# Optimization experiments

Measured on AMD Instinct MI355X. Metric: run time of the kernel, lower is better.

Reference implementation:

```python
import jax, jax.numpy as jnp
import numpy as np

B, G, N, C = 8, 16, 1024, 256


def setup_inputs() -> dict:
    key = jax.random.key(0)
    k1, k2, k3, k4, k5 = jax.random.split(key, 5)
    x = jax.random.normal(k1, (B, G, N, C), dtype=jnp.float32)
    vs = jax.random.normal(k2, (B, G, 1, N, 3), dtype=jnp.float32)
    s = 1.0 / np.sqrt(C)
    W_fc = jax.random.normal(k3, (C, C), dtype=jnp.float32) * s   # nn.Linear weight [out,in]
    b_fc = jax.random.normal(k4, (C,), dtype=jnp.float32) * s
    W_vn = jax.random.normal(k5, (C, C), dtype=jnp.float32) * s   # VNLinear weight [out,in], no bias
    return {"x": x, "vs": vs, "W_fc": W_fc, "b_fc": b_fc, "W_vn": W_vn}


def reference(x, vs, W_fc, b_fc, W_vn):
    # q = fc(x): [B,G,N,C]
    q = jnp.einsum('bgnc,oc->bgno', x, W_fc) + b_fc
    # softmax over the point dim N (torch dim=2)
    atten = jax.nn.softmax(q, axis=2)
    xw = atten * x  # [B,G,N,C]
    # torch: expand to [B,G,C,N,3] * vs then sum over N.
    # Equivalent contraction without materializing the 5D tensor:
    v = jnp.squeeze(vs, axis=2)  # [B,G,N,3]
    out = jnp.einsum('bgnc,bgnd->bgcd', xw, v)  # [B,G,C,3]
    # VNLinear: bias-free linear over channel dim, shared across the 3 vector comps
    return jnp.einsum('bgcd,oc->bgod', out, W_vn)  # [B,G,C,3]
```

## Files before the change

### kernel.cpp

```cpp
#include <hip/hip_runtime.h>
#include <hip/hip_bf16.h>


#define NQ 1024
#define CQ 256
#define RT 32
#define TILES 8
#define WB_OFF 131072

typedef __attribute__((ext_vector_type(8))) short bf16x8;
typedef __attribute__((ext_vector_type(4))) float f32x4;

__device__ __forceinline__ ushort2 pk2(float a, float b) {
    __hip_bfloat162 h = __float22bfloat162_rn(make_float2(a, b));
    ushort2 r;
    __builtin_memcpy(&r, &h, sizeof(r));
    return r;
}

__device__ __forceinline__ void gload16(const float* g, float* l) {
    __builtin_amdgcn_global_load_lds(
        (const __attribute__((address_space(1))) unsigned int*)g,
        (__attribute__((address_space(3))) unsigned int*)l, 16, 0, 0);
}

__global__ __launch_bounds__(256)
void wfc_cvt(const float* __restrict__ Wfc, ushort* __restrict__ WbT) {
    const int i = blockIdx.x * 256 + threadIdx.x;
    const int o = i >> 6;
    const int k4 = (i & 63) * 4;
    float4 v = *reinterpret_cast<const float4*>(Wfc + (size_t)o * CQ + k4);
    ushort2 a0 = pk2(v.x, v.y), a1 = pk2(v.z, v.w);
    ushort4 pk = { a0.x, a0.y, a1.x, a1.y };
    *reinterpret_cast<ushort4*>(WbT + ((size_t)(k4 >> 3) * CQ + o) * 8 + (k4 & 7)) = pk;
}

__global__ __launch_bounds__(512, 2)
void attn_pool_partial(const float* __restrict__ x, const float* __restrict__ vs,
                       const ushort* __restrict__ WbT, float* __restrict__ ws) {
    __shared__ __align__(16) float xsf[2][RT * CQ];
    __shared__ __align__(16) float vsm[TILES * RT * 3];

    const int t = threadIdx.x;
    const int id = blockIdx.x;
    const int bg = id >> 2;
    const int ntg = id & 3;
    const int nb = ntg * (TILES * RT);

    const int w = t >> 6, lane = t & 63;
    const int quad = lane >> 4, l16 = lane & 15;
    const int sxA = (l16 & 7) << 2;

    const float* xb = x + (size_t)bg * NQ * CQ;
    const float* vb = vs + (size_t)bg * NQ * 3;

    bf16x8 Bf0[8], Bf1[8];
    const int bcol0 = w * 32 + l16;
    #pragma unroll
    for (int ks = 0; ks < 8; ++ks) {
        const size_t fo = (size_t)(ks * 4 + quad) * (CQ * 8);
        Bf0[ks] = *reinterpret_cast<const bf16x8*>(WbT + fo + (size_t)bcol0 * 8);
        Bf1[ks] = *reinterpret_cast<const bf16x8*>(WbT + fo + (size_t)(bcol0 + 16) * 8);
    }
    __builtin_amdgcn_sched_barrier(0);

    const bool vload = (t < 192);
    float4 vreg;
    if (vload) vreg = reinterpret_cast<const float4*>(vb + (size_t)nb * 3)[t];
    __builtin_amdgcn_sched_barrier(0);

    #pragma unroll
    for (int p = 0; p < 4; ++p) {
        const int row = p * 8 + w;
        gload16(xb + (size_t)(nb + row) * CQ + (((lane * 4) ^ (w << 2))),
                &xsf[0][row * CQ]);
    }
    __builtin_amdgcn_sched_barrier(0);
    if (vload) reinterpret_cast<float4*>(vsm)[t] = vreg;
    __builtin_amdgcn_sched_barrier(0);
    asm volatile("s_waitcnt vmcnt(0) lgkmcnt(0)" ::: "memory");
    __builtin_amdgcn_sched_barrier(0);
    __builtin_amdgcn_s_barrier();
    __builtin_amdgcn_sched_barrier(0);

    float rZ[2] = {0.f, 0.f}, rS0[2] = {0.f, 0.f}, rS1[2] = {0.f, 0.f}, rS2[2] = {0.f, 0.f};

    for (int i = 0; i < TILES; ++i) {
        const int cur = i & 1;
        const float* xsb = xsf[cur];

        if (i < TILES - 1) {
            const size_t gr = (size_t)(nb + (i + 1) * RT);
            float* dst = xsf[cur ^ 1];
            #pragma unroll
            for (int p = 0; p < 4; ++p) {
                const int row = p * 8 + w;
                gload16(xb + (gr + row) * CQ + (((lane * 4) ^ (w << 2))),
                        dst + row * CQ);
            }
        }
        __builtin_amdgcn_sched_barrier(0);

        f32x4 acc[2][2];
        #pragma unroll
        for (int mi = 0; mi < 2; ++mi)
            #pragma unroll
            for (int ci = 0; ci < 2; ++ci) acc[mi][ci] = (f32x4){0.f, 0.f, 0.f, 0.f};

        __builtin_amdgcn_s_setprio(1);
        #pragma unroll
        for (int ks = 0; ks < 8; ++ks) {
            const int kk = ks * 32 + quad * 8;
            #pragma unroll
            for (int mi = 0; mi < 2; ++mi) {
                const int row = mi * 16 + l16;
                float4 h0 = *reinterpret_cast<const float4*>(&xsb[row * CQ + (kk ^ sxA)]);
                float4 h1 = *reinterpret_cast<const float4*>(&xsb[row * CQ + ((kk + 4) ^ sxA)]);
                ushort2 p0 = pk2(h0.x, h0.y), p1 = pk2(h0.z, h0.w);
                ushort2 p2 = pk2(h1.x, h1.y), p3 = pk2(h1.z, h1.w);
                bf16x8 a = (bf16x8){ (short)p0.x, (short)p0.y, (short)p1.x, (short)p1.y,
                                     (short)p2.x, (short)p2.y, (short)p3.x, (short)p3.y };
                acc[mi][0] = __builtin_amdgcn_mfma_f32_16x16x32_bf16(a, Bf0[ks], acc[mi][0], 0, 0, 0);
                acc[mi][1] = __builtin_amdgcn_mfma_f32_16x16x32_bf16(a, Bf1[ks], acc[mi][1], 0, 0, 0);
            }
        }
        __builtin_amdgcn_s_setprio(0);

        const float* vt = vsm + (size_t)(i * RT) * 3;
        #pragma unroll
        for (int mi = 0; mi < 2; ++mi) {
            const int rbase = mi * 16 + quad * 4;
            float v0[4], v1[4], v2[4];
            #pragma unroll
            for (int r = 0; r < 4; ++r) {
                v0[r] = vt[(rbase + r) * 3 + 0];
                v1[r] = vt[(rbase + r) * 3 + 1];
                v2[r] = vt[(rbase + r) * 3 + 2];
            }
            #pragma unroll
            for (int ci = 0; ci < 2; ++ci) {
                const int xc = w * 32 + ci * 16 + l16;
                #pragma unroll
                for (int r = 0; r < 4; ++r) {
                    const int row = rbase + r;
                    float e = __expf(acc[mi][ci][r]);
                    float xv = xsb[row * CQ + (xc ^ ((row & 7) << 2))];
                    rZ[ci] += e;
                    float p = e * xv;
                    rS0[ci] = fmaf(p, v0[r], rS0[ci]);
                    rS1[ci] = fmaf(p, v1[r], rS1[ci]);
                    rS2[ci] = fmaf(p, v2[r], rS2[ci]);
                }
            }
        }

        __builtin_amdgcn_sched_barrier(0);
        asm volatile("s_waitcnt vmcnt(0)" ::: "memory");
        __builtin_amdgcn_sched_barrier(0);
        __builtin_amdgcn_s_barrier();
        __builtin_amdgcn_sched_barrier(0);
    }

    #pragma unroll
    for (int ci = 0; ci < 2; ++ci) {
        float z = rZ[ci], s0 = rS0[ci], s1 = rS1[ci], s2 = rS2[ci];
        #pragma unroll
        for (int off = 16; off < 64; off <<= 1) {
            z  += __shfl_xor(z,  off);
            s0 += __shfl_xor(s0, off);
            s1 += __shfl_xor(s1, off);
            s2 += __shfl_xor(s2, off);
        }
        if (quad == 0) {
            const int col = w * 32 + ci * 16 + l16;
            float* p = ws + ((size_t)bg * CQ + col) * 4;
            atomicAdd(&p[0], z);
            atomicAdd(&p[1], s0);
            atomicAdd(&p[2], s1);
            atomicAdd(&p[3], s2);
        }
    }
}

__global__ __launch_bounds__(256, 4)
void vn_linear(const float* __restrict__ ws, const float* __restrict__ Wvn,
               float* __restrict__ out) {
    __shared__ float Tsm[CQ][3];
    const int bg = blockIdx.x, t = threadIdx.x;
    {
        f32x4 z4 = *reinterpret_cast<const f32x4*>(ws + ((size_t)bg * CQ + t) * 4);
        float inv = 1.f / z4[0];
        Tsm[t][0] = z4[1] * inv;
        Tsm[t][1] = z4[2] * inv;
        Tsm[t][2] = z4[3] * inv;
    }
    __syncthreads();
    const float* wr = Wvn + (size_t)t * CQ;
    float a0 = 0.f, a1 = 0.f, a2 = 0.f;
    #pragma unroll
    for (int c = 0; c < CQ; c += 4) {
        float4 w4 = *reinterpret_cast<const float4*>(wr + c);
        a0 += w4.x * Tsm[c + 0][0] + w4.y * Tsm[c + 1][0]
            + w4.z * Tsm[c + 2][0] + w4.w * Tsm[c + 3][0];
        a1 += w4.x * Tsm[c + 0][1] + w4.y * Tsm[c + 1][1]
            + w4.z * Tsm[c + 2][1] + w4.w * Tsm[c + 3][1];
        a2 += w4.x * Tsm[c + 0][2] + w4.y * Tsm[c + 1][2]
            + w4.z * Tsm[c + 2][2] + w4.w * Tsm[c + 3][2];
    }
    float* op = out + ((size_t)bg * CQ + t) * 3;
    op[0] = a0; op[1] = a1; op[2] = a2;
}

extern "C" void kernel_launch(void* const* d_in, const int* in_sizes, int n_in,
                              void* d_out, int out_size, void* d_ws, size_t ws_size,
                              hipStream_t stream) {
    const float* x   = (const float*)d_in[0];
    const float* vs  = (const float*)d_in[1];
    const float* Wfc = (const float*)d_in[2];
    const float* Wvn = (const float*)d_in[4];
    float* out = (float*)d_out;
    float* ws  = (float*)d_ws;

    ushort* WbT = (ushort*)(ws + WB_OFF);

    (void)hipMemsetAsync(ws, 0, (size_t)128 * CQ * 4 * sizeof(float), stream);
    wfc_cvt<<<dim3(64), dim3(256), 0, stream>>>(Wfc, WbT);
    attn_pool_partial<<<dim3(512), dim3(512), 0, stream>>>(x, vs, WbT, ws);
    vn_linear<<<dim3(128), dim3(256), 0, stream>>>(ws, Wvn, out);
}
```

Measured before the change: 221.1 us.

## Convert x tiles to bf16 once in LDS before MFMA consumption

Each x tile now lands as fp32 in a single staging buffer, is converted once to bf16 into a swizzled double-buffered bf16 tile, and the MFMA A-fragments are loaded directly as bf16x8. This removes the conversions every wave repeated on the same rows and halves LDS read traffic for the A operand. In exchange it adds an extra LDS write/read pass and an extra barrier per tile, serialises the prefetch through one landing buffer, and the x values used in the pooling sum are now rounded to bf16, which changes accuracy.

Measured after the change: 216.7 us. 1.02x faster.

```diff
diff --git a/kernel.cpp b/kernel.cpp
--- a/kernel.cpp
+++ b/kernel.cpp
@@ -17,11 +17,23 @@
     __builtin_memcpy(&r, &h, sizeof(r));
     return r;
 }
+__device__ __forceinline__ float bf2f(ushort h) {
+    union { unsigned u; float f; } v; v.u = ((unsigned)h) << 16;
+    return v.f;
+}
 
 __device__ __forceinline__ void gload16(const float* g, float* l) {
     __builtin_amdgcn_global_load_lds(
         (const __attribute__((address_space(1))) unsigned int*)g,
         (__attribute__((address_space(3))) unsigned int*)l, 16, 0, 0);
+}
+
+__device__ __forceinline__ void bar_lgkm() {
+    __builtin_amdgcn_sched_barrier(0);
+    asm volatile("s_waitcnt lgkmcnt(0)" ::: "memory");
+    __builtin_amdgcn_sched_barrier(0);
+    __builtin_amdgcn_s_barrier();
+    __builtin_amdgcn_sched_barrier(0);
 }
 
 __global__ __launch_bounds__(256)
@@ -38,7 +50,8 @@
 __global__ __launch_bounds__(512, 2)
 void attn_pool_partial(const float* __restrict__ x, const float* __restrict__ vs,
                        const ushort* __restrict__ WbT, float* __restrict__ ws) {
-    __shared__ __align__(16) float xsf[2][RT * CQ];
+    __shared__ __align__(16) float land[RT * CQ];
+    __shared__ __align__(16) char  bx[2][RT * 512];
     __shared__ __align__(16) float vsm[TILES * RT * 3];
 
     const int t = threadIdx.x;
@@ -49,7 +62,6 @@
 
     const int w = t >> 6, lane = t & 63;
     const int quad = lane >> 4, l16 = lane & 15;
-    const int sxA = (l16 & 7) << 2;
 
     const float* xb = x + (size_t)bg * NQ * CQ;
     const float* vb = vs + (size_t)bg * NQ * 3;
@@ -72,31 +84,38 @@
     #pragma unroll
     for (int p = 0; p < 4; ++p) {
         const int row = p * 8 + w;
-        gload16(xb + (size_t)(nb + row) * CQ + (((lane * 4) ^ (w << 2))),
-                &xsf[0][row * CQ]);
-    }
+        gload16(xb + (size_t)(nb + row) * CQ + lane * 4, &land[row * CQ]);
+    }
+    __builtin_amdgcn_sched_barrier(0);
+    asm volatile("s_waitcnt vmcnt(0)" ::: "memory");
     __builtin_amdgcn_sched_barrier(0);
     if (vload) reinterpret_cast<float4*>(vsm)[t] = vreg;
-    __builtin_amdgcn_sched_barrier(0);
-    asm volatile("s_waitcnt vmcnt(0) lgkmcnt(0)" ::: "memory");
-    __builtin_amdgcn_sched_barrier(0);
-    __builtin_amdgcn_s_barrier();
-    __builtin_amdgcn_sched_barrier(0);
+    bar_lgkm();
+
+    {
+        char* dst = bx[0];
+        #pragma unroll
+        for (int p = 0; p < 4; ++p) {
+            const int row = p * 8 + w;
+            float4 v4 = *reinterpret_cast<const float4*>(&land[row * CQ + lane * 4]);
+            ushort2 a0 = pk2(v4.x, v4.y), a1 = pk2(v4.z, v4.w);
+            ushort4 pk = { a0.x, a0.y, a1.x, a1.y };
+            *reinterpret_cast<ushort4*>(dst + row * 512 + ((lane * 8) ^ ((row & 7) << 4))) = pk;
+        }
+    }
+    bar_lgkm();
 
     float rZ[2] = {0.f, 0.f}, rS0[2] = {0.f, 0.f}, rS1[2] = {0.f, 0.f}, rS2[2] = {0.f, 0.f};
 
     for (int i = 0; i < TILES; ++i) {
-        const int cur = i & 1;
-        const float* xsb = xsf[cur];
+        const char* bxp = bx[i & 1];
 
         if (i < TILES - 1) {
-            const size_t gr = (size_t)(nb + (i + 1) * RT);
-            float* dst = xsf[cur ^ 1];
+            const int tb = nb + (i + 1) * RT;
             #pragma unroll
             for (int p = 0; p < 4; ++p) {
                 const int row = p * 8 + w;
-                gload16(xb + (gr + row) * CQ + (((lane * 4) ^ (w << 2))),
-                        dst + row * CQ);
+                gload16(xb + (size_t)(tb + row) * CQ + lane * 4, &land[row * CQ]);
             }
         }
         __builtin_amdgcn_sched_barrier(0);
@@ -110,16 +129,12 @@
         __builtin_amdgcn_s_setprio(1);
         #pragma unroll
         for (int ks = 0; ks < 8; ++ks) {
-            const int kk = ks * 32 + quad * 8;
+            const int kkb = ks * 64 + quad * 16;
             #pragma unroll
             for (int mi = 0; mi < 2; ++mi) {
                 const int row = mi * 16 + l16;
-                float4 h0 = *reinterpret_cast<const float4*>(&xsb[row * CQ + (kk ^ sxA)]);
-                float4 h1 = *reinterpret_cast<const float4*>(&xsb[row * CQ + ((kk + 4) ^ sxA)]);
-                ushort2 p0 = pk2(h0.x, h0.y), p1 = pk2(h0.z, h0.w);
-                ushort2 p2 = pk2(h1.x, h1.y), p3 = pk2(h1.z, h1.w);
-                bf16x8 a = (bf16x8){ (short)p0.x, (short)p0.y, (short)p1.x, (short)p1.y,
-                                     (short)p2.x, (short)p2.y, (short)p3.x, (short)p3.y };
+                bf16x8 a = *reinterpret_cast<const bf16x8*>(
+                    bxp + row * 512 + (kkb ^ ((row & 7) << 4)));
                 acc[mi][0] = __builtin_amdgcn_mfma_f32_16x16x32_bf16(a, Bf0[ks], acc[mi][0], 0, 0, 0);
                 acc[mi][1] = __builtin_amdgcn_mfma_f32_16x16x32_bf16(a, Bf1[ks], acc[mi][1], 0, 0, 0);
             }
@@ -144,7 +159,9 @@
                 for (int r = 0; r < 4; ++r) {
                     const int row = rbase + r;
                     float e = __expf(acc[mi][ci][r]);
-                    float xv = xsb[row * CQ + (xc ^ ((row & 7) << 2))];
+                    ushort h = *reinterpret_cast<const ushort*>(
+                        bxp + row * 512 + ((xc * 2) ^ ((row & 7) << 4)));
+                    float xv = bf2f(h);
                     rZ[ci] += e;
                     float p = e * xv;
                     rS0[ci] = fmaf(p, v0[r], rS0[ci]);
@@ -159,6 +176,19 @@
         __builtin_amdgcn_sched_barrier(0);
         __builtin_amdgcn_s_barrier();
         __builtin_amdgcn_sched_barrier(0);
+
+        if (i < TILES - 1) {
+            char* dst = bx[(i + 1) & 1];
+            #pragma unroll
+            for (int p = 0; p < 4; ++p) {
+                const int row = p * 8 + w;
+                float4 v4 = *reinterpret_cast<const float4*>(&land[row * CQ + lane * 4]);
+                ushort2 a0 = pk2(v4.x, v4.y), a1 = pk2(v4.z, v4.w);
+                ushort4 pk = { a0.x, a0.y, a1.x, a1.y };
+                *reinterpret_cast<ushort4*>(dst + row * 512 + ((lane * 8) ^ ((row & 7) << 4))) = pk;
+            }
+            bar_lgkm();
+        }
     }
 
     #pragma unroll
```
